# Kernel optimization log

Measured on AMD Instinct MI355X. Metric: run time of the kernel, lower is better.

The kernel has to match this reference:

```python
import jax, jax.numpy as jnp
import numpy as np

N_NODES = 100000
N_EDGES = 3200000  # avg degree 32
NFEAT = 512
NOUT = 7
DIMS = [NFEAT, 12, 10, 8, 6, 4, NOUT]  # hard-coded hidden widths from __init__


def setup_inputs() -> dict:
    key = jax.random.key(0)
    ks = jax.random.split(key, 4 + 2 * 6)
    inp = {
        "x": jax.random.normal(ks[0], (N_NODES, NFEAT), dtype=jnp.float32),
        "edge_val": jax.random.uniform(ks[1], (N_EDGES,), dtype=jnp.float32) / 32.0,  # ~normalized adj
        "edge_src": jax.random.randint(ks[2], (N_EDGES,), 0, N_NODES),
        "edge_dst": jax.random.randint(ks[3], (N_EDGES,), 0, N_NODES),
    }
    for i in range(6):
        s = 1.0 / np.sqrt(DIMS[i + 1])  # pygcn reset_parameters: U(-1/sqrt(out), 1/sqrt(out))
        inp[f"W{i+1}"] = jax.random.uniform(ks[4 + 2 * i], (DIMS[i], DIMS[i + 1]), jnp.float32, -s, s)
        inp[f"b{i+1}"] = jax.random.uniform(ks[5 + 2 * i], (DIMS[i + 1],), jnp.float32, -s, s)
    return inp


def reference(x, edge_val, W1, b1, W2, b2, W3, b3, W4, b4, W5, b5, W6, b6,
              edge_src, edge_dst):
    n = x.shape[0]

    def gc(h, W, b):
        s = h @ W                                   # [N, out] dense mm
        m = edge_val[:, None] * s[edge_src]         # gather + scale per edge
        agg = jax.ops.segment_sum(m, edge_dst, num_segments=n)  # spmm scatter
        return agg + b

    tanhshrink = lambda v: v - jnp.tanh(v)

    h = gc(x, W1, b1)                # dropout p=0 -> identity
    h = jax.nn.relu(gc(h, W2, b2))   # eval-mode dropout -> identity
    h = tanhshrink(gc(h, W3, b3))
    h = tanhshrink(gc(h, W4, b4))
    h = gc(h, W5, b5)
    return gc(h, W6, b6)
```

## Files before the change

### kernel.cpp

```cpp
#include <hip/hip_runtime.h>
#include <math.h>
#include <stdint.h>


#define T_EDGES 12800
#define NB_MAX  1600
#define FCAP    2560

__global__ __launch_bounds__(512) void hist_kernel(const int* __restrict__ dst,
                                                   int* __restrict__ ghist, int E, int NB) {
    __shared__ int h[NB_MAX];
    for (int i = threadIdx.x; i < NB; i += 512) h[i] = 0;
    __syncthreads();
    int base = blockIdx.x * T_EDGES;
    int n = min(T_EDGES, E - base);
    for (int i = threadIdx.x; i < n; i += 512)
        atomicAdd(&h[((unsigned)dst[base + i]) >> 6], 1);
    __syncthreads();
    for (int i = threadIdx.x; i < NB; i += 512)
        ghist[(size_t)blockIdx.x * NB + i] = h[i];
}

__global__ __launch_bounds__(256) void scanA_kernel(const int* __restrict__ ghist,
                                                    int* __restrict__ btot, int NT, int NB) {
    __shared__ int red[256];
    int b = blockIdx.x, t = threadIdx.x;
    int s = 0;
    for (int tt = t; tt < NT; tt += 256) s += ghist[(size_t)tt * NB + b];
    red[t] = s;
    __syncthreads();
    for (int off = 128; off > 0; off >>= 1) {
        if (t < off) red[t] += red[t + off];
        __syncthreads();
    }
    if (t == 0) btot[b] = red[0];
}

__global__ __launch_bounds__(256) void scanB_kernel(const int* __restrict__ btot,
                                                    int* __restrict__ bbase,
                                                    int* __restrict__ bucket_ptr, int NB) {
    __shared__ int part[256];
    int t = threadIdx.x;
    int chunk = (NB + 255) / 256;
    int lo = t * chunk, hi = min(lo + chunk, NB);
    int s = 0;
    for (int i = lo; i < hi; i++) s += btot[i];
    part[t] = s;
    __syncthreads();
    for (int off = 1; off < 256; off <<= 1) {
        int x = (t >= off) ? part[t - off] : 0;
        __syncthreads();
        part[t] += x;
        __syncthreads();
    }
    int run = part[t] - s;
    for (int i = lo; i < hi; i++) {
        bbase[i] = run;
        bucket_ptr[i] = run;
        run += btot[i];
    }
    if (t == 255) bucket_ptr[NB] = run;
}

__global__ __launch_bounds__(256) void scanC_kernel(const int* __restrict__ ghist,
                                                    const int* __restrict__ bbase,
                                                    int* __restrict__ goff, int NT, int NB) {
    __shared__ int part[256];
    int b = blockIdx.x, t = threadIdx.x;
    int v = (t < NT) ? ghist[(size_t)t * NB + b] : 0;
    part[t] = v;
    __syncthreads();
    for (int off = 1; off < 256; off <<= 1) {
        int x = (t >= off) ? part[t - off] : 0;
        __syncthreads();
        part[t] += x;
        __syncthreads();
    }
    if (t < NT) goff[(size_t)t * NB + b] = bbase[b] + part[t] - v;
}

__global__ __launch_bounds__(1024) void scatter_kernel(const int* __restrict__ src,
                                                       const int* __restrict__ dst,
                                                       const float* __restrict__ val,
                                                       const int* __restrict__ ghist,
                                                       const int* __restrict__ goff,
                                                       int2* __restrict__ edges, int E, int NB) {
    __shared__ unsigned perm[T_EDGES];
    __shared__ int loff[NB_MAX];
    __shared__ int lcur[NB_MAX];
    __shared__ int part[1024];
    int tb = blockIdx.x, t = threadIdx.x;
    int base = tb * T_EDGES;
    int n = min(T_EDGES, E - base);

    int chunk = (NB + 1023) / 1024;
    int lo = t * chunk, hi = min(lo + chunk, NB);
    int s = 0;
    for (int i = lo; i < hi; i++) {
        int c = ghist[(size_t)tb * NB + i];
        loff[i] = c;
        s += c;
    }
    part[t] = s;
    __syncthreads();
    for (int off = 1; off < 1024; off <<= 1) {
        int x = (t >= off) ? part[t - off] : 0;
        __syncthreads();
        part[t] += x;
        __syncthreads();
    }
    int run = part[t] - s;
    for (int i = lo; i < hi; i++) {
        int c = loff[i];
        loff[i] = run;
        lcur[i] = run;
        run += c;
    }
    __syncthreads();

    for (int i = t; i < n; i += 1024) {
        int d = dst[base + i];
        unsigned b = ((unsigned)d) >> 6;
        int p = atomicAdd(&lcur[b], 1);
        perm[p] = (unsigned)i | (b << 14) | ((unsigned)(d & 63) << 25);
    }
    __syncthreads();

    for (int o = t; o < n; o += 1024) {
        unsigned v = perm[o];
        int li = v & 16383;
        int b  = (v >> 14) & 2047;
        int ld = v >> 25;
        int g  = goff[(size_t)tb * NB + b] + (o - loff[b]);
        edges[g] = make_int2(src[base + li] | (ld << 17), __float_as_int(val[base + li]));
    }
}

__global__ __launch_bounds__(512) void finalize_kernel(int2* __restrict__ edges,
                                                       const int* __restrict__ bucket_ptr) {
    __shared__ int2 recs[FCAP];
    __shared__ int2 recs2[FCAP];
    __shared__ int cnt[64], offs[64], cur[64];
    int b = blockIdx.x, t = threadIdx.x;
    int s0 = bucket_ptr[b], s1 = bucket_ptr[b + 1];
    int ne = min(s1 - s0, FCAP);
    if (t < 64) cnt[t] = 0;
    __syncthreads();
    for (int i = t; i < ne; i += 512) {
        int2 r = edges[s0 + i];
        recs[i] = r;
        atomicAdd(&cnt[(r.x >> 17) & 63], 1);
    }
    __syncthreads();
    if (t == 0) {
        int run = 0;
        for (int i = 0; i < 64; i++) { offs[i] = run; run += cnt[i]; }
    }
    __syncthreads();
    if (t < 64) cur[t] = offs[t];
    __syncthreads();
    for (int i = t; i < ne; i += 512) {
        int2 r = recs[i];
        int ld = (r.x >> 17) & 63;
        int p = atomicAdd(&cur[ld], 1);
        recs2[p] = r;
    }
    __syncthreads();
    for (int i = t; i < ne; i += 512) edges[s0 + i] = recs2[i];
}

__global__ __launch_bounds__(256) void dense1_kernel(const float* __restrict__ x,
                                                     const float* __restrict__ W,
                                                     float* __restrict__ out, int N) {
    __shared__ float xs[256 * 33];
    const int t    = threadIdx.x;
    const int row0 = blockIdx.x * 256;
    const int r    = row0 + t;

    float acc[12];
#pragma unroll
    for (int j = 0; j < 12; j++) acc[j] = 0.f;

    for (int tile = 0; tile < 16; ++tile) {
#pragma unroll
        for (int i = 0; i < 8; i++) {
            int idx4 = t + 256 * i;
            int flat = idx4 * 4;
            int rl   = flat >> 5;
            int c    = flat & 31;
            int rg   = row0 + rl;
            if (rg >= N) rg = N - 1;
            const float4 v = *(const float4*)(x + (size_t)rg * 512 + tile * 32 + c);
            float* p = &xs[rl * 33 + c];
            p[0] = v.x; p[1] = v.y; p[2] = v.z; p[3] = v.w;
        }
        __syncthreads();
#pragma unroll 8
        for (int kk = 0; kk < 32; ++kk) {
            float xv = xs[t * 33 + kk];
            int k = tile * 32 + kk;
#pragma unroll
            for (int j = 0; j < 12; j++) acc[j] += xv * W[k * 12 + j];
        }
        __syncthreads();
    }
    if (r < N) {
#pragma unroll
        for (int j = 0; j < 12; j++) out[(size_t)r * 12 + j] = acc[j];
    }
}

template <int NV, int DIN, int DOUT, int OSTR, int ACT, bool FINAL>
__global__ __launch_bounds__(256) void layer_kernel(const int2* __restrict__ edges,
                                                    const int* __restrict__ bucket_ptr,
                                                    const float* __restrict__ s,
                                                    const float* __restrict__ bias,
                                                    const float* __restrict__ W,
                                                    float* __restrict__ out, int N) {
    constexpr int ASTR = 13;
    __shared__ int2  ebuf[FCAP];
    __shared__ float acc[64 * ASTR];
    const int b = blockIdx.x, t = threadIdx.x;
    const int s0 = bucket_ptr[b];
    const int ne = min(bucket_ptr[b + 1] - s0, FCAP);

    for (int i = t; i < 64 * ASTR; i += 256) acc[i] = 0.f;
    for (int i = t; i < ne; i += 256) ebuf[i] = edges[s0 + i];
    __syncthreads();

    const int K  = (ne + 255) >> 8;
    const int i0 = t * K;
    const int i1 = min(i0 + K, ne);
    if (i0 < i1) {
        const float4* sv = (const float4*)s;
        float4 a[NV];
#pragma unroll
        for (int v = 0; v < NV; v++) a[v] = make_float4(0.f, 0.f, 0.f, 0.f);
        int cd = (ebuf[i0].x >> 17) & 63;
        for (int i = i0; i < i1; ++i) {
            int2 ev = ebuf[i];
            int ld = (ev.x >> 17) & 63;
            if (ld != cd) {
#pragma unroll
                for (int v = 0; v < NV; v++) {
                    atomicAdd(&acc[cd * ASTR + 4 * v + 0], a[v].x);
                    atomicAdd(&acc[cd * ASTR + 4 * v + 1], a[v].y);
                    atomicAdd(&acc[cd * ASTR + 4 * v + 2], a[v].z);
                    atomicAdd(&acc[cd * ASTR + 4 * v + 3], a[v].w);
                    a[v] = make_float4(0.f, 0.f, 0.f, 0.f);
                }
                cd = ld;
            }
            float w = __int_as_float(ev.y);
            const float4* srow = sv + (size_t)(ev.x & 0x1FFFF) * NV;
#pragma unroll
            for (int v = 0; v < NV; v++) {
                float4 xr = srow[v];
                a[v].x += w * xr.x; a[v].y += w * xr.y;
                a[v].z += w * xr.z; a[v].w += w * xr.w;
            }
        }
#pragma unroll
        for (int v = 0; v < NV; v++) {
            atomicAdd(&acc[cd * ASTR + 4 * v + 0], a[v].x);
            atomicAdd(&acc[cd * ASTR + 4 * v + 1], a[v].y);
            atomicAdd(&acc[cd * ASTR + 4 * v + 2], a[v].z);
            atomicAdd(&acc[cd * ASTR + 4 * v + 3], a[v].w);
        }
    }
    __syncthreads();

    if (t < 64) {
        int node = (b << 6) + t;
        if (node < N) {
            float h[DIN];
#pragma unroll
            for (int k = 0; k < DIN; k++) {
                float z = acc[t * ASTR + k] + bias[k];
                if (ACT == 1) z = fmaxf(z, 0.f);
                else if (ACT == 2) z = z - tanhf(z);
                h[k] = z;
            }
            if (FINAL) {
#pragma unroll
                for (int k = 0; k < DIN; k++) out[(size_t)node * DIN + k] = h[k];
            } else {
                float o[OSTR];
#pragma unroll
                for (int j = 0; j < OSTR; j++) o[j] = 0.f;
#pragma unroll
                for (int j = 0; j < DOUT; j++) {
                    float tj = 0.f;
#pragma unroll
                    for (int k = 0; k < DIN; k++) tj += h[k] * W[k * DOUT + j];
                    o[j] = tj;
                }
                float4* orow = (float4*)(out + (size_t)node * OSTR);
#pragma unroll
                for (int v = 0; v < OSTR / 4; v++)
                    orow[v] = make_float4(o[4 * v], o[4 * v + 1], o[4 * v + 2], o[4 * v + 3]);
            }
        }
    }
}


static inline size_t align256(size_t x) { return (x + 255) & ~(size_t)255; }

extern "C" void kernel_launch(void* const* d_in, const int* in_sizes, int n_in,
                              void* d_out, int out_size, void* d_ws, size_t ws_size,
                              hipStream_t stream) {
    const float* x        = (const float*)d_in[0];
    const float* edge_val = (const float*)d_in[1];
    const int*   edge_src = (const int*)d_in[2];
    const int*   edge_dst = (const int*)d_in[3];
    const float* W1 = (const float*)d_in[4];   const float* b1 = (const float*)d_in[5];
    const float* W2 = (const float*)d_in[6];   const float* b2 = (const float*)d_in[7];
    const float* W3 = (const float*)d_in[8];   const float* b3 = (const float*)d_in[9];
    const float* W4 = (const float*)d_in[10];  const float* b4 = (const float*)d_in[11];
    const float* W5 = (const float*)d_in[12];  const float* b5 = (const float*)d_in[13];
    const float* W6 = (const float*)d_in[14];  const float* b6 = (const float*)d_in[15];

    const int N = in_sizes[0] / 512;
    const int E = in_sizes[1];
    float* out = (float*)d_out;

    const int NB = (N + 63) >> 6;
    const int NT = (E + T_EDGES - 1) / T_EDGES;
    const int nb = (N + 255) / 256;

    char* w = (char*)d_ws;
    float* A          = (float*)w;  w += align256((size_t)N * 12 * sizeof(float));
    float* B          = (float*)w;  w += align256((size_t)N * 12 * sizeof(float));
    int*   ghist      = (int*)w;    w += align256((size_t)NT * NB * sizeof(int));
    int*   goff       = (int*)w;    w += align256((size_t)NT * NB * sizeof(int));
    int*   btot       = (int*)w;    w += align256((size_t)NB * sizeof(int));
    int*   bbase      = (int*)w;    w += align256((size_t)NB * sizeof(int));
    int*   bucket_ptr = (int*)w;    w += align256((size_t)(NB + 1) * sizeof(int));
    int2*  edges      = (int2*)w;   w += align256((size_t)E * sizeof(int2));

    hist_kernel<<<NT, 512, 0, stream>>>(edge_dst, ghist, E, NB);
    scanA_kernel<<<NB, 256, 0, stream>>>(ghist, btot, NT, NB);
    scanB_kernel<<<1, 256, 0, stream>>>(btot, bbase, bucket_ptr, NB);
    scanC_kernel<<<NB, 256, 0, stream>>>(ghist, bbase, goff, NT, NB);
    scatter_kernel<<<NT, 1024, 0, stream>>>(edge_src, edge_dst, edge_val, ghist, goff, edges, E, NB);
    finalize_kernel<<<NB, 512, 0, stream>>>(edges, bucket_ptr);

    dense1_kernel<<<nb, 256, 0, stream>>>(x, W1, A, N);

    layer_kernel<3, 12, 10, 12, 0, false><<<NB, 256, 0, stream>>>(edges, bucket_ptr, A, b1, W2, B, N);
    layer_kernel<3, 10, 8, 8, 1, false><<<NB, 256, 0, stream>>>(edges, bucket_ptr, B, b2, W3, A, N);
    layer_kernel<2, 8, 6, 8, 2, false><<<NB, 256, 0, stream>>>(edges, bucket_ptr, A, b3, W4, B, N);
    layer_kernel<2, 6, 4, 4, 2, false><<<NB, 256, 0, stream>>>(edges, bucket_ptr, B, b4, W5, A, N);
    layer_kernel<1, 4, 7, 8, 0, false><<<NB, 256, 0, stream>>>(edges, bucket_ptr, A, b5, W6, B, N);
    layer_kernel<2, 7, 7, 8, 0, true><<<NB, 256, 0, stream>>>(edges, bucket_ptr, B, b6, (const float*)nullptr, out, N);
}
```

Measured before the change: 726.9 us.

## Use fixed-capacity bucket slots, drop global scan, and balance edge work via per-node chunks

Each 64-node bucket now gets a fixed FCAP-sized slot in the edge array. This removes the global scanA/scanB kernels and the bucket_ptr prefix, and scanC writes per-bucket totals directly. Finalize emits a per-bucket table of per-node offsets. The layer kernel uses that table to split each node's edges into fixed-length chunks of up to 10 and distributes the chunks across threads, replacing contiguous per-thread ranges that crossed node boundaries. The 12-wide feature rows are padded to 16 floats so they can be stored and loaded as float4. The trade-offs are more workspace, wasted lanes in partially filled chunks, and reliance on no bucket exceeding FCAP edges.

Result: no change. 728.2 us (+0.2%).

```diff
diff --git a/kernel.cpp b/kernel.cpp
--- a/kernel.cpp
+++ b/kernel.cpp
@@ -6,6 +6,9 @@
 #define T_EDGES 12800
 #define NB_MAX  1600
 #define FCAP    2560
+#define OTSTR   72
+#define KIT     10
+#define MAXIT   336
 
 __global__ __launch_bounds__(512) void hist_kernel(const int* __restrict__ dst,
                                                    int* __restrict__ ghist, int E, int NB) {
@@ -21,50 +24,9 @@
         ghist[(size_t)blockIdx.x * NB + i] = h[i];
 }
 
-__global__ __launch_bounds__(256) void scanA_kernel(const int* __restrict__ ghist,
+__global__ __launch_bounds__(256) void scanC_kernel(const int* __restrict__ ghist,
+                                                    int* __restrict__ goff,
                                                     int* __restrict__ btot, int NT, int NB) {
-    __shared__ int red[256];
-    int b = blockIdx.x, t = threadIdx.x;
-    int s = 0;
-    for (int tt = t; tt < NT; tt += 256) s += ghist[(size_t)tt * NB + b];
-    red[t] = s;
-    __syncthreads();
-    for (int off = 128; off > 0; off >>= 1) {
-        if (t < off) red[t] += red[t + off];
-        __syncthreads();
-    }
-    if (t == 0) btot[b] = red[0];
-}
-
-__global__ __launch_bounds__(256) void scanB_kernel(const int* __restrict__ btot,
-                                                    int* __restrict__ bbase,
-                                                    int* __restrict__ bucket_ptr, int NB) {
-    __shared__ int part[256];
-    int t = threadIdx.x;
-    int chunk = (NB + 255) / 256;
-    int lo = t * chunk, hi = min(lo + chunk, NB);
-    int s = 0;
-    for (int i = lo; i < hi; i++) s += btot[i];
-    part[t] = s;
-    __syncthreads();
-    for (int off = 1; off < 256; off <<= 1) {
-        int x = (t >= off) ? part[t - off] : 0;
-        __syncthreads();
-        part[t] += x;
-        __syncthreads();
-    }
-    int run = part[t] - s;
-    for (int i = lo; i < hi; i++) {
-        bbase[i] = run;
-        bucket_ptr[i] = run;
-        run += btot[i];
-    }
-    if (t == 255) bucket_ptr[NB] = run;
-}
-
-__global__ __launch_bounds__(256) void scanC_kernel(const int* __restrict__ ghist,
-                                                    const int* __restrict__ bbase,
-                                                    int* __restrict__ goff, int NT, int NB) {
     __shared__ int part[256];
     int b = blockIdx.x, t = threadIdx.x;
     int v = (t < NT) ? ghist[(size_t)t * NB + b] : 0;
@@ -76,7 +38,8 @@
         part[t] += x;
         __syncthreads();
     }
-    if (t < NT) goff[(size_t)t * NB + b] = bbase[b] + part[t] - v;
+    if (t < NT) goff[(size_t)t * NB + b] = b * FCAP + part[t] - v;
+    if (t == 255) btot[b] = part[255];
 }
 
 __global__ __launch_bounds__(1024) void scatter_kernel(const int* __restrict__ src,
@@ -137,13 +100,14 @@
 }
 
 __global__ __launch_bounds__(512) void finalize_kernel(int2* __restrict__ edges,
-                                                       const int* __restrict__ bucket_ptr) {
+                                                       const int* __restrict__ btot,
+                                                       int* __restrict__ offsTab) {
     __shared__ int2 recs[FCAP];
     __shared__ int2 recs2[FCAP];
     __shared__ int cnt[64], offs[64], cur[64];
     int b = blockIdx.x, t = threadIdx.x;
-    int s0 = bucket_ptr[b], s1 = bucket_ptr[b + 1];
-    int ne = min(s1 - s0, FCAP);
+    size_t s0 = (size_t)b * FCAP;
+    int ne = min(btot[b], FCAP);
     if (t < 64) cnt[t] = 0;
     __syncthreads();
     for (int i = t; i < ne; i += 512) {
@@ -167,6 +131,8 @@
     }
     __syncthreads();
     for (int i = t; i < ne; i += 512) edges[s0 + i] = recs2[i];
+    if (t < 64) offsTab[(size_t)b * OTSTR + t] = offs[t];
+    if (t == 64) offsTab[(size_t)b * OTSTR + 64] = ne;
 }
 
 __global__ __launch_bounds__(256) void dense1_kernel(const float* __restrict__ x,
@@ -205,14 +171,17 @@
         __syncthreads();
     }
     if (r < N) {
-#pragma unroll
-        for (int j = 0; j < 12; j++) out[(size_t)r * 12 + j] = acc[j];
-    }
-}
-
-template <int NV, int DIN, int DOUT, int OSTR, int ACT, bool FINAL>
+        float4* orow = (float4*)(out + (size_t)r * 16);
+        orow[0] = make_float4(acc[0], acc[1], acc[2], acc[3]);
+        orow[1] = make_float4(acc[4], acc[5], acc[6], acc[7]);
+        orow[2] = make_float4(acc[8], acc[9], acc[10], acc[11]);
+        orow[3] = make_float4(0.f, 0.f, 0.f, 0.f);
+    }
+}
+
+template <int SV, int ANV, int DIN, int DOUT, int OSTR, int ACT, bool FINAL>
 __global__ __launch_bounds__(256) void layer_kernel(const int2* __restrict__ edges,
-                                                    const int* __restrict__ bucket_ptr,
+                                                    const int* __restrict__ offsTab,
                                                     const float* __restrict__ s,
                                                     const float* __restrict__ bias,
                                                     const float* __restrict__ W,
@@ -220,52 +189,61 @@
     constexpr int ASTR = 13;
     __shared__ int2  ebuf[FCAP];
     __shared__ float acc[64 * ASTR];
+    __shared__ int   offs[65];
+    __shared__ int   items[MAXIT];
+    __shared__ int   nitems_s;
     const int b = blockIdx.x, t = threadIdx.x;
-    const int s0 = bucket_ptr[b];
-    const int ne = min(bucket_ptr[b + 1] - s0, FCAP);
+    const int ne = offsTab[(size_t)b * OTSTR + 64];
 
     for (int i = t; i < 64 * ASTR; i += 256) acc[i] = 0.f;
-    for (int i = t; i < ne; i += 256) ebuf[i] = edges[s0 + i];
-    __syncthreads();
-
-    const int K  = (ne + 255) >> 8;
-    const int i0 = t * K;
-    const int i1 = min(i0 + K, ne);
-    if (i0 < i1) {
-        const float4* sv = (const float4*)s;
-        float4 a[NV];
-#pragma unroll
-        for (int v = 0; v < NV; v++) a[v] = make_float4(0.f, 0.f, 0.f, 0.f);
-        int cd = (ebuf[i0].x >> 17) & 63;
-        for (int i = i0; i < i1; ++i) {
-            int2 ev = ebuf[i];
-            int ld = (ev.x >> 17) & 63;
-            if (ld != cd) {
-#pragma unroll
-                for (int v = 0; v < NV; v++) {
-                    atomicAdd(&acc[cd * ASTR + 4 * v + 0], a[v].x);
-                    atomicAdd(&acc[cd * ASTR + 4 * v + 1], a[v].y);
-                    atomicAdd(&acc[cd * ASTR + 4 * v + 2], a[v].z);
-                    atomicAdd(&acc[cd * ASTR + 4 * v + 3], a[v].w);
-                    a[v] = make_float4(0.f, 0.f, 0.f, 0.f);
-                }
-                cd = ld;
+    for (int i = t; i < ne; i += 256) ebuf[i] = edges[(size_t)b * FCAP + i];
+    if (t < 65) offs[t] = offsTab[(size_t)b * OTSTR + t];
+    if (t == 0) nitems_s = 0;
+    __syncthreads();
+
+    if (t < 64) {
+        int st = offs[t];
+        int c  = ((t == 63) ? ne : offs[t + 1]) - st;
+        if (c > 0) {
+            int ni  = (c + KIT - 1) / KIT;
+            int pos = atomicAdd(&nitems_s, ni);
+            for (int j = 0; j < ni; j++) {
+                int len = min(KIT, c - j * KIT);
+                items[pos + j] = ((st + j * KIT) << 10) | (len << 6) | t;
             }
-            float w = __int_as_float(ev.y);
-            const float4* srow = sv + (size_t)(ev.x & 0x1FFFF) * NV;
-#pragma unroll
-            for (int v = 0; v < NV; v++) {
+        }
+    }
+    __syncthreads();
+
+    const int nit = nitems_s;
+    const float4* sv = (const float4*)s;
+    for (int j = t; j < nit; j += 256) {
+        int it = items[j];
+        int ld    = it & 63;
+        int lenm1 = ((it >> 6) & 15) - 1;
+        int st    = it >> 10;
+        float4 a[ANV];
+#pragma unroll
+        for (int v = 0; v < ANV; v++) a[v] = make_float4(0.f, 0.f, 0.f, 0.f);
+#pragma unroll
+        for (int k = 0; k < KIT; k++) {
+            int idx = st + min(k, lenm1);
+            int2 ev = ebuf[idx];
+            float w = (k <= lenm1) ? __int_as_float(ev.y) : 0.f;
+            const float4* srow = sv + (size_t)(ev.x & 0x1FFFF) * SV;
+#pragma unroll
+            for (int v = 0; v < ANV; v++) {
                 float4 xr = srow[v];
                 a[v].x += w * xr.x; a[v].y += w * xr.y;
                 a[v].z += w * xr.z; a[v].w += w * xr.w;
             }
         }
 #pragma unroll
-        for (int v = 0; v < NV; v++) {
-            atomicAdd(&acc[cd * ASTR + 4 * v + 0], a[v].x);
-            atomicAdd(&acc[cd * ASTR + 4 * v + 1], a[v].y);
-            atomicAdd(&acc[cd * ASTR + 4 * v + 2], a[v].z);
-            atomicAdd(&acc[cd * ASTR + 4 * v + 3], a[v].w);
+        for (int v = 0; v < ANV; v++) {
+            atomicAdd(&acc[ld * ASTR + 4 * v + 0], a[v].x);
+            atomicAdd(&acc[ld * ASTR + 4 * v + 1], a[v].y);
+            atomicAdd(&acc[ld * ASTR + 4 * v + 2], a[v].z);
+            atomicAdd(&acc[ld * ASTR + 4 * v + 3], a[v].w);
         }
     }
     __syncthreads();
@@ -330,28 +308,25 @@
     const int nb = (N + 255) / 256;
 
     char* w = (char*)d_ws;
-    float* A          = (float*)w;  w += align256((size_t)N * 12 * sizeof(float));
-    float* B          = (float*)w;  w += align256((size_t)N * 12 * sizeof(float));
-    int*   ghist      = (int*)w;    w += align256((size_t)NT * NB * sizeof(int));
-    int*   goff       = (int*)w;    w += align256((size_t)NT * NB * sizeof(int));
-    int*   btot       = (int*)w;    w += align256((size_t)NB * sizeof(int));
-    int*   bbase      = (int*)w;    w += align256((size_t)NB * sizeof(int));
-    int*   bucket_ptr = (int*)w;    w += align256((size_t)(NB + 1) * sizeof(int));
-    int2*  edges      = (int2*)w;   w += align256((size_t)E * sizeof(int2));
+    float* A       = (float*)w;  w += align256((size_t)N * 16 * sizeof(float));
+    float* B       = (float*)w;  w += align256((size_t)N * 16 * sizeof(float));
+    int*   ghist   = (int*)w;    w += align256((size_t)NT * NB * sizeof(int));
+    int*   goff    = (int*)w;    w += align256((size_t)NT * NB * sizeof(int));
+    int*   btot    = (int*)w;    w += align256((size_t)NB * sizeof(int));
+    int*   offsTab = (int*)w;    w += align256((size_t)NB * OTSTR * sizeof(int));
+    int2*  edges   = (int2*)w;   w += align256((size_t)NB * FCAP * sizeof(int2));
 
     hist_kernel<<<NT, 512, 0, stream>>>(edge_dst, ghist, E, NB);
-    scanA_kernel<<<NB, 256, 0, stream>>>(ghist, btot, NT, NB);
-    scanB_kernel<<<1, 256, 0, stream>>>(btot, bbase, bucket_ptr, NB);
-    scanC_kernel<<<NB, 256, 0, stream>>>(ghist, bbase, goff, NT, NB);
+    scanC_kernel<<<NB, 256, 0, stream>>>(ghist, goff, btot, NT, NB);
     scatter_kernel<<<NT, 1024, 0, stream>>>(edge_src, edge_dst, edge_val, ghist, goff, edges, E, NB);
-    finalize_kernel<<<NB, 512, 0, stream>>>(edges, bucket_ptr);
+    finalize_kernel<<<NB, 512, 0, stream>>>(edges, btot, offsTab);
 
     dense1_kernel<<<nb, 256, 0, stream>>>(x, W1, A, N);
 
-    layer_kernel<3, 12, 10, 12, 0, false><<<NB, 256, 0, stream>>>(edges, bucket_ptr, A, b1, W2, B, N);
-    layer_kernel<3, 10, 8, 8, 1, false><<<NB, 256, 0, stream>>>(edges, bucket_ptr, B, b2, W3, A, N);
-    layer_kernel<2, 8, 6, 8, 2, false><<<NB, 256, 0, stream>>>(edges, bucket_ptr, A, b3, W4, B, N);
-    layer_kernel<2, 6, 4, 4, 2, false><<<NB, 256, 0, stream>>>(edges, bucket_ptr, B, b4, W5, A, N);
-    layer_kernel<1, 4, 7, 8, 0, false><<<NB, 256, 0, stream>>>(edges, bucket_ptr, A, b5, W6, B, N);
-    layer_kernel<2, 7, 7, 8, 0, true><<<NB, 256, 0, stream>>>(edges, bucket_ptr, B, b6, (const float*)nullptr, out, N);
-}
+    layer_kernel<4, 3, 12, 10, 16, 0, false><<<NB, 256, 0, stream>>>(edges, offsTab, A, b1, W2, B, N);
+    layer_kernel<4, 3, 10, 8, 8, 1, false><<<NB, 256, 0, stream>>>(edges, offsTab, B, b2, W3, A, N);
+    layer_kernel<2, 2, 8, 6, 8, 2, false><<<NB, 256, 0, stream>>>(edges, offsTab, A, b3, W4, B, N);
+    layer_kernel<2, 2, 6, 4, 4, 2, false><<<NB, 256, 0, stream>>>(edges, offsTab, B, b4, W5, A, N);
+    layer_kernel<1, 1, 4, 7, 8, 0, false><<<NB, 256, 0, stream>>>(edges, offsTab, A, b5, W6, B, N);
+    layer_kernel<2, 2, 7, 7, 8, 0, true><<<NB, 256, 0, stream>>>(edges, offsTab, B, b6, (const float*)nullptr, out, N);
+}
```
